# Kernel tuning notes

Measured on AMD Instinct MI355X. Metric: run time of the kernel, lower is better.

The kernel has to match this reference:

```python
import jax, jax.numpy as jnp
import numpy as np

N_E = 1024
N_H = 16
SZ = N_E // N_H  # 64
NEG_INF = float('-inf')


def _layernorm(x, g, b):
    # Faithful to source: unbiased variance (ddof=1), eps added AFTER sqrt.
    mu = jnp.mean(x, axis=-1, keepdims=True)
    v = jnp.var(x, axis=-1, keepdims=True, ddof=1)
    xn = (x - mu) / (jnp.sqrt(v) + 1e-8)
    return g * xn + b


def setup_inputs() -> dict:
    key = jax.random.key(0)
    ks = jax.random.split(key, 16)
    s = 0.02
    x = jax.random.normal(ks[0], (4, 2048, N_E), dtype=jnp.float32)
    # Stacked per-head Q/K/V linears: weight [H, sz, n_e], bias [H, sz]
    Wq = jax.random.normal(ks[1], (N_H, SZ, N_E), dtype=jnp.float32) * s
    bq = jax.random.normal(ks[2], (N_H, SZ), dtype=jnp.float32) * s
    Wk = jax.random.normal(ks[3], (N_H, SZ, N_E), dtype=jnp.float32) * s
    bk = jax.random.normal(ks[4], (N_H, SZ), dtype=jnp.float32) * s
    Wv = jax.random.normal(ks[5], (N_H, SZ, N_E), dtype=jnp.float32) * s
    bv = jax.random.normal(ks[6], (N_H, SZ), dtype=jnp.float32) * s
    Wo = jax.random.normal(ks[7], (N_E, N_E), dtype=jnp.float32) * s
    bo = jax.random.normal(ks[8], (N_E,), dtype=jnp.float32) * s
    g1 = jnp.ones((N_E,), dtype=jnp.float32)
    be1 = jnp.zeros((N_E,), dtype=jnp.float32)
    g2 = jnp.ones((N_E,), dtype=jnp.float32)
    be2 = jnp.zeros((N_E,), dtype=jnp.float32)
    W1 = jax.random.normal(ks[9], (4 * N_E, N_E), dtype=jnp.float32) * s
    bf1 = jax.random.normal(ks[10], (4 * N_E,), dtype=jnp.float32) * s
    W2 = jax.random.normal(ks[11], (N_E, 4 * N_E), dtype=jnp.float32) * s
    bf2 = jax.random.normal(ks[12], (N_E,), dtype=jnp.float32) * s
    return dict(x=x, Wq=Wq, bq=bq, Wk=Wk, bk=bk, Wv=Wv, bv=bv, Wo=Wo, bo=bo,
                g1=g1, be1=be1, g2=g2, be2=be2, W1=W1, bf1=bf1, W2=W2, bf2=bf2)


def reference(x, Wq, bq, Wk, bk, Wv, bv, Wo, bo, g1, be1, g2, be2, W1, bf1, W2, bf2):
    # --- MHA sublayer ---
    xn = _layernorm(x, g1, be1)
    # Q/K/V for all heads at once: [B, H, S, sz]
    Q = jnp.einsum('bsd,hkd->bhsk', xn, Wq) + bq[None, :, None, :]
    K = jnp.einsum('bsd,hkd->bhsk', xn, Wk) + bk[None, :, None, :]
    V = jnp.einsum('bsd,hkd->bhsk', xn, Wv) + bv[None, :, None, :]
    scores = jnp.einsum('bhqk,bhmk->bhqm', Q, K) / (SZ ** 0.5)  # [B,H,S,S]
    # Faithful to source quirk: mask where tril(scores) == 0
    masked = jnp.where(jnp.tril(scores) == 0, NEG_INF, scores)
    attn = jax.nn.softmax(masked, axis=-1)
    o = jnp.einsum('bhqm,bhmk->bhqk', attn, V)  # [B,H,S,sz]
    B, H, S, _ = o.shape
    o = jnp.transpose(o, (0, 2, 1, 3)).reshape(B, S, H * SZ)  # concat heads
    x = x + o @ Wo.T + bo
    # --- FFN sublayer (dropout = identity in eval) ---
    xn2 = _layernorm(x, g2, be2)
    h = jax.nn.gelu(xn2 @ W1.T + bf1, approximate=False)
    x = x + h @ W2.T + bf2
    return x
```

## Files before the change

kernel.cpp:

```cpp
#include <hip/hip_runtime.h>
#include <math.h>


typedef unsigned short u16;
typedef unsigned int u32;
typedef __attribute__((ext_vector_type(8))) short bf16x8;
typedef __attribute__((ext_vector_type(4))) float f32x4;

#define T_TOK 8192
#define DM    1024
#define SEQ   2048

__device__ __forceinline__ u16 f2bf(float f) {
  union { float f; unsigned int u; } c; c.f = f;
  unsigned int u = c.u + 0x7fffu + ((c.u >> 16) & 1u);
  return (u16)(u >> 16);
}

__device__ __forceinline__ u32 pk2(float a, float b) {
  return (u32)f2bf(a) | ((u32)f2bf(b) << 16);
}

__device__ __forceinline__ float bf2f(short s) {
  union { float f; unsigned int u; } c; c.u = ((u32)(u16)s) << 16;
  return c.f;
}

__device__ __forceinline__ void gload16(const void* gp, void* lp) {
  __builtin_amdgcn_global_load_lds(
      (const __attribute__((address_space(1))) void*)gp,
      (__attribute__((address_space(3))) void*)lp, 16, 0, 0);
}

__device__ __forceinline__ float gelu_tanh(float v) {
  float u = 0.7978845608f * (v + 0.044715f * v * v * v);
  return v / (1.0f + __expf(-2.0f * u));
}

__global__ __launch_bounds__(256) void cast_all(const float* __restrict__ Wq,
    const float* __restrict__ Wk, const float* __restrict__ Wv,
    const float* __restrict__ Wo, const float* __restrict__ W1,
    const float* __restrict__ W2, u16* __restrict__ WqkvB,
    u16* __restrict__ WoB, u16* __restrict__ W1B, u16* __restrict__ W2B) {
  for (int i = blockIdx.x * 256 + threadIdx.x; i < 3145728; i += gridDim.x * 256) {
    const float* s; u16* d; int j;
    if (i < 262144)       { s = Wq; d = WqkvB;           j = i; }
    else if (i < 524288)  { s = Wk; d = WqkvB + 1048576; j = i - 262144; }
    else if (i < 786432)  { s = Wv; d = WqkvB + 2097152; j = i - 524288; }
    else if (i < 1048576) { s = Wo; d = WoB;             j = i - 786432; }
    else if (i < 2097152) { s = W1; d = W1B;             j = i - 1048576; }
    else                  { s = W2; d = W2B;             j = i - 2097152; }
    float4 v = reinterpret_cast<const float4*>(s)[j];
    ushort4 o = { f2bf(v.x), f2bf(v.y), f2bf(v.z), f2bf(v.w) };
    reinterpret_cast<ushort4*>(d)[j] = o;
  }
}

__global__ __launch_bounds__(256) void concat_bias(const float* __restrict__ q,
    const float* __restrict__ k, const float* __restrict__ v, float* __restrict__ out) {
  int i = blockIdx.x * 256 + threadIdx.x;
  float val = (i < 1024) ? q[i] : (i < 2048) ? k[i - 1024] : v[i - 2048];
  out[i] = val;
}

__global__ __launch_bounds__(256) void ln_kernel(const float* __restrict__ x,
    const float* __restrict__ g, const float* __restrict__ b, u16* __restrict__ out) {
  __shared__ float red[4];
  const int tid = threadIdx.x, l = tid & 63, w = tid >> 6;
  const size_t row = blockIdx.x;
  float4 v = reinterpret_cast<const float4*>(x + row * DM)[tid];
  float s = v.x + v.y + v.z + v.w;
#pragma unroll
  for (int off = 1; off < 64; off <<= 1) s += __shfl_xor(s, off, 64);
  if (l == 0) red[w] = s;
  __syncthreads();
  float mu = (red[0] + red[1] + red[2] + red[3]) * (1.0f / 1024.0f);
  float dx = v.x - mu, dy = v.y - mu, dz = v.z - mu, dw = v.w - mu;
  float ss = dx * dx + dy * dy + dz * dz + dw * dw;
#pragma unroll
  for (int off = 1; off < 64; off <<= 1) ss += __shfl_xor(ss, off, 64);
  __syncthreads();
  if (l == 0) red[w] = ss;
  __syncthreads();
  float var = (red[0] + red[1] + red[2] + red[3]) * (1.0f / 1023.0f);
  float inv = 1.0f / (sqrtf(var) + 1e-8f);
  const int c = tid * 4;
  u16* o = out + row * DM + c;
  o[0] = f2bf(dx * inv * g[c + 0] + b[c + 0]);
  o[1] = f2bf(dy * inv * g[c + 1] + b[c + 1]);
  o[2] = f2bf(dz * inv * g[c + 2] + b[c + 2]);
  o[3] = f2bf(dw * inv * g[c + 3] + b[c + 3]);
}

__global__ __launch_bounds__(256) void vt_kernel(const u16* __restrict__ vr,
                                                 u16* __restrict__ vt) {
  __shared__ u16 t[64][72];
  const int st = blockIdx.x;
  const int bh = blockIdx.y, b = bh >> 4, h = bh & 15;
  const int tid = threadIdx.x;
  const int ss = tid >> 3, dc = (tid & 7) * 8;
  const u16* src = vr + (size_t)(b * SEQ + st * 64) * 1024 + h * 64;
  *(bf16x8*)&t[ss][dc]      = *(const bf16x8*)(src + (size_t)ss * 1024 + dc);
  *(bf16x8*)&t[ss + 32][dc] = *(const bf16x8*)(src + (size_t)(ss + 32) * 1024 + dc);
  __syncthreads();
  const int d0 = tid >> 3, s0 = (tid & 7) * 8;
  u16* dst = vt + (size_t)bh * 64 * SEQ + st * 64;
  bf16x8 o0, o1;
#pragma unroll
  for (int i = 0; i < 8; ++i) {
    o0[i] = (short)t[s0 + i][d0];
    o1[i] = (short)t[s0 + i][d0 + 32];
  }
  *(bf16x8*)(dst + (size_t)d0 * SEQ + s0)        = o0;
  *(bf16x8*)(dst + (size_t)(d0 + 32) * SEQ + s0) = o1;
}

template <int EPI, int BM>
__global__ __launch_bounds__(512) void gemm8p(const u16* __restrict__ A,
    const u16* __restrict__ Bw, const float* __restrict__ bias,
    const float* res, void* Cout, void* aux, int M, int N, int K, int gx) {
  constexpr int MI  = BM / 32;
  constexpr int AMI = MI / 2;
  constexpr int VC  = (BM == 256) ? 6 : 5;
  __shared__ __align__(16) u16 ldsA[2][2][BM * 32];
  __shared__ __align__(16) u16 ldsB[2][2][256 * 32];
  const int tid = threadIdx.x;
  const int l = tid & 63;
  const int w = tid >> 6;
  const int wm = w >> 2, wn = w & 3;
  const int lr = l & 15, lg = l >> 4;

  const int nb = gridDim.x;
  const int q = nb >> 3, r = nb & 7;
  const int xcd = blockIdx.x & 7, jj = blockIdx.x >> 3;
  const int lid = (xcd < r ? xcd * (q + 1) : r * (q + 1) + (xcd - r) * q) + jj;
  const int stid = lid >> 5, pos = lid & 31;
  const int nstx = gx >> 2;
  const int stx = stid % nstx, sty = stid / nstx;
  const int bx = stx * 4 + (pos & 3), by = sty * 8 + (pos >> 2);
  const int m0 = by * BM, n0 = bx * 256;

  const int Dl = tid * 16;
  const int Ls = Dl ^ (((Dl >> 7) & 3) << 4);
  const int srow = Ls >> 6;
  const int scol = (Ls & 63) >> 1;
  const u16* aS0 = A  + (size_t)(m0 + srow) * K + scol;
  const u16* aS1 = aS0 + (size_t)128 * K;
  const u16* bS0 = Bw + (size_t)(n0 + srow) * K + scol;
  const u16* bS1 = bS0 + (size_t)128 * K;

  const int sx = ((lr >> 1) & 3) << 4;
  const int aBase = (wm * (BM / 2) + lr) * 64 + ((lg * 16) ^ sx);
  const int bBase = (wn * 64 + lr) * 64 + ((lg * 16) ^ sx);

  f32x4 acc[MI][4];
#pragma unroll
  for (int i = 0; i < MI; ++i)
#pragma unroll
    for (int j = 0; j < 4; ++j) acc[i][j] = f32x4{0.f, 0.f, 0.f, 0.f};
  bf16x8 bv[2][4];

  const int NT = K >> 6;
  const int NI = NT >> 1;

  auto stA = [&](int d, int ks, int tile) {
    u16* dst = &ldsA[d][ks][tid * 8];
    const int ko = tile * 64 + ks * 32;
    gload16(aS0 + ko, dst);
    if constexpr (BM == 256) gload16(aS1 + ko, dst + 4096);
  };
  auto stB = [&](int d, int ks, int tile) {
    u16* dst = &ldsB[d][ks][tid * 8];
    const int ko = tile * 64 + ks * 32;
    gload16(bS0 + ko, dst);
    gload16(bS1 + ko, dst + 4096);
  };

  stB(0, 0, 0); stB(0, 1, 0); stA(0, 0, 0); stA(0, 1, 0);
  stB(1, 0, 1); stB(1, 1, 1); stA(1, 0, 1);
  asm volatile("s_waitcnt vmcnt(%0)" :: "i"(VC) : "memory");
  __builtin_amdgcn_sched_barrier(0);
  __builtin_amdgcn_s_barrier();

#define PHASE(DBUF, KS, MH, READB, STAGE, ENDV)                               \
  {                                                                           \
    const char* abuf = (const char*)&ldsA[DBUF][KS][0];                       \
    const char* bbuf = (const char*)&ldsB[DBUF][KS][0];                       \
    bf16x8 av[AMI];                                                           \
    _Pragma("unroll")                                                         \
    for (int i = 0; i < AMI; ++i)                                             \
      av[i] = *(const bf16x8*)(abuf + aBase + ((MH) * AMI + i) * 1024);       \
    if (READB) {                                                              \
      _Pragma("unroll")                                                       \
      for (int ni = 0; ni < 4; ++ni)                                          \
        bv[KS][ni] = *(const bf16x8*)(bbuf + bBase + ni * 1024);              \
    }                                                                         \
    STAGE;                                                                    \
    __builtin_amdgcn_s_barrier();                                             \
    asm volatile("s_waitcnt lgkmcnt(0)" ::: "memory");                        \
    __builtin_amdgcn_sched_barrier(0);                                        \
    __builtin_amdgcn_s_setprio(1);                                            \
    _Pragma("unroll")                                                         \
    for (int i = 0; i < AMI; ++i)                                             \
      _Pragma("unroll")                                                       \
      for (int ni = 0; ni < 4; ++ni)                                          \
        acc[(MH) * AMI + i][ni] = __builtin_amdgcn_mfma_f32_16x16x32_bf16(    \
            av[i], bv[KS][ni], acc[(MH) * AMI + i][ni], 0, 0, 0);             \
    __builtin_amdgcn_s_setprio(0);                                            \
    ENDV;                                                                     \
    __builtin_amdgcn_s_barrier();                                             \
  }

#define ENDV_CNT                                                              \
  {                                                                           \
    if (t + 1 < NI) {                                                         \
      asm volatile("s_waitcnt vmcnt(%0)" :: "i"(VC) : "memory");              \
    } else {                                                                  \
      asm volatile("s_waitcnt vmcnt(0)" ::: "memory");                        \
    }                                                                         \
    __builtin_amdgcn_sched_barrier(0);                                        \
  }

  for (int t = 0; t < NI; ++t) {
    const int t2 = 2 * t;
    const bool s0 = (t2 + 2 < NT);
    const bool s1 = (t2 + 3 < NT);
    PHASE(0, 0, 0, 1, { stA(1, 1, t2 + 1); }, {});
    PHASE(0, 1, 0, 1, { if (s0) stB(0, 0, t2 + 2); }, {});
    PHASE(0, 0, 1, 0, { if (s0) stB(0, 1, t2 + 2); }, {});
    PHASE(0, 1, 1, 0, { if (s0) stA(0, 0, t2 + 2); }, ENDV_CNT);
    PHASE(1, 0, 0, 1, { if (s0) stA(0, 1, t2 + 2); }, {});
    PHASE(1, 1, 0, 1, { if (s1) stB(1, 0, t2 + 3); }, {});
    PHASE(1, 0, 1, 0, { if (s1) stB(1, 1, t2 + 3); }, {});
    PHASE(1, 1, 1, 0, { if (s1) stA(1, 0, t2 + 3); }, ENDV_CNT);
  }
#undef PHASE
#undef ENDV_CNT

  float bs[4];
#pragma unroll
  for (int ni = 0; ni < 4; ++ni) bs[ni] = bias[n0 + wn * 64 + ni * 16 + lr];
#pragma unroll
  for (int mi = 0; mi < MI; ++mi) {
#pragma unroll
    for (int j = 0; j < 4; ++j) {
      const int rr = m0 + wm * (BM / 2) + mi * 16 + lg * 4 + j;
#pragma unroll
      for (int ni = 0; ni < 4; ++ni) {
        const int c = n0 + wn * 64 + ni * 16 + lr;
        float v = acc[mi][ni][j] + bs[ni];
        if constexpr (EPI == 0) {
          if (n0 >= 2048) {
            ((u16*)aux)[(size_t)rr * 1024 + (c - 2048)] = f2bf(v);
          } else {
            ((u16*)Cout)[(size_t)rr * 2048 + c] = f2bf(v);
          }
        } else if constexpr (EPI == 1) {
          const size_t idx = (size_t)rr * N + c;
          ((float*)Cout)[idx] = v + res[idx];
        } else {
          const size_t idx = (size_t)rr * N + c;
          ((u16*)Cout)[idx] = f2bf(gelu_tanh(v));
        }
      }
    }
  }
}

__global__ __launch_bounds__(512) void attn_kernel(const u16* __restrict__ qk,
    const u16* __restrict__ vt, u16* __restrict__ obuf) {
  __shared__ __align__(16) u16 ldsK[3][64 * 64];
  __shared__ __align__(16) u16 ldsV[3][64 * 64];
  __shared__ __align__(16) u16 ldsP[8][2][16 * 72];
  const int tid = threadIdx.x, l = tid & 63, w = tid >> 6;
  const int lr = l & 15, lg = l >> 4;
  const int bx = blockIdx.x;
  const int bh = blockIdx.y, b = bh >> 4, h = bh & 15;
  const u16* qbase = qk + (size_t)b * SEQ * 2048 + h * 64;
  const u16* kbase = qk + (size_t)b * SEQ * 2048 + 1024 + h * 64;
  const u16* vbase = vt + (size_t)bh * 64 * SEQ;

  const int srow = tid >> 3;
  const int scb  = ((tid & 7) * 16) ^ ((srow & 7) << 4);
  const int sel  = scb >> 1;

  auto stageKV = [&](int t) {
    const int bi = t % 3;
    gload16(kbase + (size_t)(t * 64 + srow) * 2048 + sel, &ldsK[bi][tid * 8]);
    gload16(vbase + (size_t)srow * SEQ + t * 64 + sel,    &ldsV[bi][tid * 8]);
  };

#pragma unroll
  for (int half = 0; half < 2; ++half) {
    const int qt = half ? (7 - bx) : bx;
    const int q0 = qt * 256 + w * 32;
    bf16x8 qf[2][2];
#pragma unroll
    for (int mi = 0; mi < 2; ++mi)
#pragma unroll
      for (int ks = 0; ks < 2; ++ks) {
        bf16x8 raw = *(const bf16x8*)(qbase +
            (size_t)(q0 + mi * 16 + lr) * 2048 + ks * 32 + lg * 8);
        bf16x8 sc8;
#pragma unroll
        for (int i = 0; i < 8; ++i) sc8[i] = (short)f2bf(bf2f(raw[i]) * 0.125f);
        qf[mi][ks] = sc8;
      }

    f32x4 o[2][4];
#pragma unroll
    for (int mi = 0; mi < 2; ++mi)
#pragma unroll
      for (int nd = 0; nd < 4; ++nd) o[mi][nd] = f32x4{0.f, 0.f, 0.f, 0.f};
    float m_[2] = {-1e30f, -1e30f}, ls[2] = {0.f, 0.f};

    const int nt = 4 * qt + 4;
    const int qmaxw = q0 + 31;

    stageKV(0);

    for (int kt = 0; kt < nt; ++kt) {
      if (kt + 1 < nt) {
        stageKV(kt + 1);
        asm volatile("s_waitcnt vmcnt(2)" ::: "memory");
      } else {
        asm volatile("s_waitcnt vmcnt(0)" ::: "memory");
      }
      __builtin_amdgcn_s_barrier();
      __builtin_amdgcn_sched_barrier(0);
      const u16* bK = &ldsK[kt % 3][0];
      const u16* bV = &ldsV[kt % 3][0];

      if (kt * 64 <= qmaxw) {
        f32x4 sc[2][4];
#pragma unroll
        for (int mi = 0; mi < 2; ++mi)
#pragma unroll
          for (int ni = 0; ni < 4; ++ni) sc[mi][ni] = f32x4{0.f, 0.f, 0.f, 0.f};
#pragma unroll
        for (int ks = 0; ks < 2; ++ks)
#pragma unroll
          for (int ni = 0; ni < 4; ++ni) {
            const int r2 = ni * 16 + lr;
            const int cb = (r2 << 7) + ((ks * 64 + lg * 16) ^ ((r2 & 7) << 4));
            bf16x8 kf = *(const bf16x8*)&bK[cb >> 1];
            sc[0][ni] = __builtin_amdgcn_mfma_f32_16x16x32_bf16(kf, qf[0][ks], sc[0][ni], 0, 0, 0);
            sc[1][ni] = __builtin_amdgcn_mfma_f32_16x16x32_bf16(kf, qf[1][ks], sc[1][ni], 0, 0, 0);
          }

        if (kt * 64 + 63 > q0) {
#pragma unroll
          for (int mi = 0; mi < 2; ++mi) {
            const int qa = q0 + mi * 16 + lr;
#pragma unroll
            for (int ni = 0; ni < 4; ++ni)
#pragma unroll
              for (int j = 0; j < 4; ++j) {
                const int ka = kt * 64 + ni * 16 + lg * 4 + j;
                if (ka > qa) sc[mi][ni][j] = -1e30f;
              }
          }
        }

#pragma unroll
        for (int mi = 0; mi < 2; ++mi) {
          float mx = sc[mi][0][0];
#pragma unroll
          for (int ni = 0; ni < 4; ++ni)
#pragma unroll
            for (int j = 0; j < 4; ++j) mx = fmaxf(mx, sc[mi][ni][j]);
          mx = fmaxf(mx, __shfl_xor(mx, 16, 64));
          mx = fmaxf(mx, __shfl_xor(mx, 32, 64));
          const float newm = fmaxf(m_[mi], mx);
          const float alpha = __expf(m_[mi] - newm);
          m_[mi] = newm;
          float ps = 0.f;
#pragma unroll
          for (int ni = 0; ni < 4; ++ni) {
            float p0 = __expf(sc[mi][ni][0] - newm);
            float p1 = __expf(sc[mi][ni][1] - newm);
            float p2 = __expf(sc[mi][ni][2] - newm);
            float p3 = __expf(sc[mi][ni][3] - newm);
            ps += (p0 + p1) + (p2 + p3);
            u32 w0 = pk2(p0, p1), w1 = pk2(p2, p3);
            *(uint2*)&ldsP[w][mi][lr * 72 + ni * 16 + lg * 4] = make_uint2(w0, w1);
          }
          ps += __shfl_xor(ps, 16, 64);
          ps += __shfl_xor(ps, 32, 64);
          ls[mi] = ls[mi] * alpha + ps;
          const float a0 = __shfl(alpha, lg * 4 + 0, 16);
          const float a1 = __shfl(alpha, lg * 4 + 1, 16);
          const float a2 = __shfl(alpha, lg * 4 + 2, 16);
          const float a3 = __shfl(alpha, lg * 4 + 3, 16);
#pragma unroll
          for (int nd = 0; nd < 4; ++nd) {
            o[mi][nd][0] *= a0; o[mi][nd][1] *= a1;
            o[mi][nd][2] *= a2; o[mi][nd][3] *= a3;
          }
        }

#pragma unroll
        for (int ks = 0; ks < 2; ++ks) {
          bf16x8 pf0 = *(const bf16x8*)&ldsP[w][0][lr * 72 + ks * 32 + lg * 8];
          bf16x8 pf1 = *(const bf16x8*)&ldsP[w][1][lr * 72 + ks * 32 + lg * 8];
#pragma unroll
          for (int nd = 0; nd < 4; ++nd) {
            const int r2 = nd * 16 + lr;
            const int cb = (r2 << 7) + ((ks * 64 + lg * 16) ^ ((r2 & 7) << 4));
            bf16x8 vf = *(const bf16x8*)&bV[cb >> 1];
            o[0][nd] = __builtin_amdgcn_mfma_f32_16x16x32_bf16(pf0, vf, o[0][nd], 0, 0, 0);
            o[1][nd] = __builtin_amdgcn_mfma_f32_16x16x32_bf16(pf1, vf, o[1][nd], 0, 0, 0);
          }
        }
      }
    }
    __builtin_amdgcn_s_barrier();

#pragma unroll
    for (int mi = 0; mi < 2; ++mi) {
      const float i0 = 1.0f / __shfl(ls[mi], lg * 4 + 0, 16);
      const float i1 = 1.0f / __shfl(ls[mi], lg * 4 + 1, 16);
      const float i2 = 1.0f / __shfl(ls[mi], lg * 4 + 2, 16);
      const float i3 = 1.0f / __shfl(ls[mi], lg * 4 + 3, 16);
      const int qrow = q0 + mi * 16 + lg * 4;
#pragma unroll
      for (int nd = 0; nd < 4; ++nd) {
        const int d = nd * 16 + lr;
        u16* op = obuf + (size_t)(b * SEQ + qrow) * DM + h * 64 + d;
        op[0 * DM] = f2bf(o[mi][nd][0] * i0);
        op[1 * DM] = f2bf(o[mi][nd][1] * i1);
        op[2 * DM] = f2bf(o[mi][nd][2] * i2);
        op[3 * DM] = f2bf(o[mi][nd][3] * i3);
      }
    }
  }
}

extern "C" void kernel_launch(void* const* d_in, const int* in_sizes, int n_in,
                              void* d_out, int out_size, void* d_ws, size_t ws_size,
                              hipStream_t stream) {
  const float* x   = (const float*)d_in[0];
  const float* Wq  = (const float*)d_in[1];
  const float* bq  = (const float*)d_in[2];
  const float* Wk  = (const float*)d_in[3];
  const float* bk  = (const float*)d_in[4];
  const float* Wv  = (const float*)d_in[5];
  const float* bv  = (const float*)d_in[6];
  const float* Wo  = (const float*)d_in[7];
  const float* bo  = (const float*)d_in[8];
  const float* g1  = (const float*)d_in[9];
  const float* be1 = (const float*)d_in[10];
  const float* g2  = (const float*)d_in[11];
  const float* be2 = (const float*)d_in[12];
  const float* W1  = (const float*)d_in[13];
  const float* bf1 = (const float*)d_in[14];
  const float* W2  = (const float*)d_in[15];
  const float* bf2 = (const float*)d_in[16];
  float* out = (float*)d_out;

  char* ws = (char*)d_ws;
  size_t off = 0;
  auto alloc = [&](size_t bytes) {
    char* p = ws + off;
    off += (bytes + 255) & ~(size_t)255;
    return p;
  };
  u16* xnB = (u16*)alloc((size_t)T_TOK * DM * 2);
  u16* D    = (u16*)alloc((size_t)T_TOK * 4096 * 2);
  u16* qkB  = D;
  u16* VTg  = D + (size_t)T_TOK * 2048;
  u16* Vrow = D + (size_t)T_TOK * 3072;
  u16* oB   = Vrow;
  u16* HB   = D;
  u16*   WqkvB = (u16*)alloc((size_t)3072 * 1024 * 2);
  u16*   WoB   = (u16*)alloc((size_t)1024 * 1024 * 2);
  u16*   W1B   = (u16*)alloc((size_t)4096 * 1024 * 2);
  u16*   W2B   = (u16*)alloc((size_t)1024 * 4096 * 2);
  float* bqkv  = (float*)alloc(3072 * 4);

  cast_all<<<2048, 256, 0, stream>>>(Wq, Wk, Wv, Wo, W1, W2,
                                     WqkvB, WoB, W1B, W2B);
  concat_bias<<<12, 256, 0, stream>>>(bq, bk, bv, bqkv);

  ln_kernel<<<T_TOK, 256, 0, stream>>>(x, g1, be1, xnB);
  gemm8p<0, 256><<<384, 512, 0, stream>>>(xnB, WqkvB, bqkv, nullptr,
                                          qkB, Vrow, T_TOK, 3072, 1024, 12);
  vt_kernel<<<dim3(32, 64), 256, 0, stream>>>(Vrow, VTg);
  attn_kernel<<<dim3(4, 64), 512, 0, stream>>>(qkB, VTg, oB);
  gemm8p<1, 128><<<256, 512, 0, stream>>>(oB, WoB, bo, x,
                                          out, nullptr, T_TOK, 1024, 1024, 4);

  ln_kernel<<<T_TOK, 256, 0, stream>>>(out, g2, be2, xnB);
  gemm8p<2, 256><<<512, 512, 0, stream>>>(xnB, W1B, bf1, nullptr,
                                          HB, nullptr, T_TOK, 4096, 1024, 16);
  gemm8p<1, 128><<<256, 512, 0, stream>>>(HB, W2B, bf2, out,
                                          out, nullptr, T_TOK, 1024, 4096, 4);
}
```

Baseline: 396.4 us.

## Transpose PV MFMA output, skip lazy softmax rescale, remap attention block order

Swaps the MFMA operand order in the P·V product so each lane owns a full query row. The per-row alpha and inverse-sum values then no longer need cross-lane shuffles, and output rows are written as packed 4-element stores. It adds a lazy max update that skips the rescale of the accumulator when the new max is within a threshold of the running max. It also pads the P staging stride to reduce LDS bank conflicts and remaps block indices to a 1D grid with interleaved ordering. The lazy threshold lets exponent values grow up to e^8 before rescaling, which slightly changes numerics.

```diff
diff --git a/kernel.cpp b/kernel.cpp
--- a/kernel.cpp
+++ b/kernel.cpp
@@ -10,6 +10,7 @@
 #define T_TOK 8192
 #define DM    1024
 #define SEQ   2048
+#define PST   88
 
 __device__ __forceinline__ u16 f2bf(float f) {
   union { float f; unsigned int u; } c; c.f = f;
@@ -271,11 +272,12 @@
     const u16* __restrict__ vt, u16* __restrict__ obuf) {
   __shared__ __align__(16) u16 ldsK[3][64 * 64];
   __shared__ __align__(16) u16 ldsV[3][64 * 64];
-  __shared__ __align__(16) u16 ldsP[8][2][16 * 72];
+  __shared__ __align__(16) u16 ldsP[8][2][16 * PST];
   const int tid = threadIdx.x, l = tid & 63, w = tid >> 6;
   const int lr = l & 15, lg = l >> 4;
-  const int bx = blockIdx.x;
-  const int bh = blockIdx.y, b = bh >> 4, h = bh & 15;
+  const int lid = (blockIdx.x & 7) * 32 + (blockIdx.x >> 3);
+  const int bh = lid >> 2, bx = lid & 3;
+  const int b = bh >> 4, h = bh & 15;
   const u16* qbase = qk + (size_t)b * SEQ * 2048 + h * 64;
   const u16* kbase = qk + (size_t)b * SEQ * 2048 + 1024 + h * 64;
   const u16* vbase = vt + (size_t)bh * 64 * SEQ;
@@ -371,45 +373,44 @@
             for (int j = 0; j < 4; ++j) mx = fmaxf(mx, sc[mi][ni][j]);
           mx = fmaxf(mx, __shfl_xor(mx, 16, 64));
           mx = fmaxf(mx, __shfl_xor(mx, 32, 64));
-          const float newm = fmaxf(m_[mi], mx);
-          const float alpha = __expf(m_[mi] - newm);
-          m_[mi] = newm;
+          if (!__all(mx <= m_[mi] + 8.0f)) {
+            const float newm = fmaxf(m_[mi], mx);
+            const float alpha = __expf(m_[mi] - newm);
+            m_[mi] = newm;
+            ls[mi] *= alpha;
+#pragma unroll
+            for (int nd = 0; nd < 4; ++nd) {
+              o[mi][nd][0] *= alpha; o[mi][nd][1] *= alpha;
+              o[mi][nd][2] *= alpha; o[mi][nd][3] *= alpha;
+            }
+          }
           float ps = 0.f;
 #pragma unroll
           for (int ni = 0; ni < 4; ++ni) {
-            float p0 = __expf(sc[mi][ni][0] - newm);
-            float p1 = __expf(sc[mi][ni][1] - newm);
-            float p2 = __expf(sc[mi][ni][2] - newm);
-            float p3 = __expf(sc[mi][ni][3] - newm);
+            float p0 = __expf(sc[mi][ni][0] - m_[mi]);
+            float p1 = __expf(sc[mi][ni][1] - m_[mi]);
+            float p2 = __expf(sc[mi][ni][2] - m_[mi]);
+            float p3 = __expf(sc[mi][ni][3] - m_[mi]);
             ps += (p0 + p1) + (p2 + p3);
             u32 w0 = pk2(p0, p1), w1 = pk2(p2, p3);
-            *(uint2*)&ldsP[w][mi][lr * 72 + ni * 16 + lg * 4] = make_uint2(w0, w1);
+            *(uint2*)&ldsP[w][mi][lr * PST + ni * 16 + lg * 4] = make_uint2(w0, w1);
           }
           ps += __shfl_xor(ps, 16, 64);
           ps += __shfl_xor(ps, 32, 64);
-          ls[mi] = ls[mi] * alpha + ps;
-          const float a0 = __shfl(alpha, lg * 4 + 0, 16);
-          const float a1 = __shfl(alpha, lg * 4 + 1, 16);
-          const float a2 = __shfl(alpha, lg * 4 + 2, 16);
-          const float a3 = __shfl(alpha, lg * 4 + 3, 16);
-#pragma unroll
-          for (int nd = 0; nd < 4; ++nd) {
-            o[mi][nd][0] *= a0; o[mi][nd][1] *= a1;
-            o[mi][nd][2] *= a2; o[mi][nd][3] *= a3;
-          }
+          ls[mi] += ps;
         }
 
 #pragma unroll
         for (int ks = 0; ks < 2; ++ks) {
-          bf16x8 pf0 = *(const bf16x8*)&ldsP[w][0][lr * 72 + ks * 32 + lg * 8];
-          bf16x8 pf1 = *(const bf16x8*)&ldsP[w][1][lr * 72 + ks * 32 + lg * 8];
+          bf16x8 pf0 = *(const bf16x8*)&ldsP[w][0][lr * PST + ks * 32 + lg * 8];
+          bf16x8 pf1 = *(const bf16x8*)&ldsP[w][1][lr * PST + ks * 32 + lg * 8];
 #pragma unroll
           for (int nd = 0; nd < 4; ++nd) {
             const int r2 = nd * 16 + lr;
             const int cb = (r2 << 7) + ((ks * 64 + lg * 16) ^ ((r2 & 7) << 4));
             bf16x8 vf = *(const bf16x8*)&bV[cb >> 1];
-            o[0][nd] = __builtin_amdgcn_mfma_f32_16x16x32_bf16(pf0, vf, o[0][nd], 0, 0, 0);
-            o[1][nd] = __builtin_amdgcn_mfma_f32_16x16x32_bf16(pf1, vf, o[1][nd], 0, 0, 0);
+            o[0][nd] = __builtin_amdgcn_mfma_f32_16x16x32_bf16(vf, pf0, o[0][nd], 0, 0, 0);
+            o[1][nd] = __builtin_amdgcn_mfma_f32_16x16x32_bf16(vf, pf1, o[1][nd], 0, 0, 0);
           }
         }
       }
@@ -418,19 +419,14 @@
 
 #pragma unroll
     for (int mi = 0; mi < 2; ++mi) {
-      const float i0 = 1.0f / __shfl(ls[mi], lg * 4 + 0, 16);
-      const float i1 = 1.0f / __shfl(ls[mi], lg * 4 + 1, 16);
-      const float i2 = 1.0f / __shfl(ls[mi], lg * 4 + 2, 16);
-      const float i3 = 1.0f / __shfl(ls[mi], lg * 4 + 3, 16);
-      const int qrow = q0 + mi * 16 + lg * 4;
+      const float inv = 1.0f / ls[mi];
+      const int qrow = q0 + mi * 16 + lr;
+      u16* op = obuf + (size_t)(b * SEQ + qrow) * DM + h * 64 + lg * 4;
 #pragma unroll
       for (int nd = 0; nd < 4; ++nd) {
-        const int d = nd * 16 + lr;
-        u16* op = obuf + (size_t)(b * SEQ + qrow) * DM + h * 64 + d;
-        op[0 * DM] = f2bf(o[mi][nd][0] * i0);
-        op[1 * DM] = f2bf(o[mi][nd][1] * i1);
-        op[2 * DM] = f2bf(o[mi][nd][2] * i2);
-        op[3 * DM] = f2bf(o[mi][nd][3] * i3);
+        ushort4 pk = { f2bf(o[mi][nd][0] * inv), f2bf(o[mi][nd][1] * inv),
+                       f2bf(o[mi][nd][2] * inv), f2bf(o[mi][nd][3] * inv) };
+        *(ushort4*)(op + nd * 16) = pk;
       }
     }
   }
@@ -486,7 +482,7 @@
   gemm8p<0, 256><<<384, 512, 0, stream>>>(xnB, WqkvB, bqkv, nullptr,
                                           qkB, Vrow, T_TOK, 3072, 1024, 12);
   vt_kernel<<<dim3(32, 64), 256, 0, stream>>>(Vrow, VTg);
-  attn_kernel<<<dim3(4, 64), 512, 0, stream>>>(qkB, VTg, oB);
+  attn_kernel<<<256, 512, 0, stream>>>(qkB, VTg, oB);
   gemm8p<1, 128><<<256, 512, 0, stream>>>(oB, WoB, bo, x,
                                           out, nullptr, T_TOK, 1024, 1024, 4);
 
```

After: 387.9 us. 1.02x faster.
